# Optimization experiments

Hardware: AMD Instinct MI355X
Metric: run time of the kernel (lower is better)

The kernel has to match this reference:

```python
import jax, jax.numpy as jnp
import numpy as np

N_NODES = 50000


def setup_inputs() -> dict:
    key = jax.random.key(0)
    k1, k2, k3, k4, k5 = jax.random.split(key, 5)
    d_in, d_out, n_edges = 128, 128, 800000
    x = jax.random.normal(k1, (N_NODES, d_in), dtype=jnp.float32)
    edge_index = jax.random.randint(k2, (2, n_edges), 0, N_NODES, dtype=jnp.int64)
    # Glorot-ish init for linear weights, bias zeros-like small normal
    W_l = jax.random.normal(k3, (d_in, d_out), dtype=jnp.float32) / np.sqrt(d_in)
    W_r = jax.random.normal(k4, (d_in, d_out), dtype=jnp.float32) / np.sqrt(d_in)
    b = jax.random.normal(k5, (d_out,), dtype=jnp.float32) * 0.01
    return {"x": x, "edge_index": edge_index, "W_l": W_l, "W_r": W_r, "b": b}


def reference(x, edge_index, W_l, W_r, b):
    # PyG SAGEConv (aggr='mean', root_weight=True, bias=True):
    #   out_i = W_l @ mean_{j: (j->i) in E} x_j + b + W_r @ x_i
    # followed by ReLU (GConv act) and dropout(p=0.0, eval) == identity.
    src, dst = edge_index[0], edge_index[1]
    msgs = x[src]                                            # [E, d_in] gather
    agg_sum = jax.ops.segment_sum(msgs, dst, num_segments=N_NODES)  # [N, d_in]
    deg = jax.ops.segment_sum(jnp.ones_like(dst, dtype=x.dtype), dst,
                              num_segments=N_NODES)          # [N]
    agg_mean = agg_sum / jnp.maximum(deg, 1.0)[:, None]      # zero for isolated nodes
    z = agg_mean @ W_l + b + x @ W_r                         # [N, d_out]
    return jax.nn.relu(z)
```

## Files before the change

### kernel.cpp

```cpp
#include <hip/hip_runtime.h>

#define N_NODES 50000
#define D 128
#define NC 256
#define SCANB 196
#define CONV_NB 1563

typedef short bf16x8 __attribute__((ext_vector_type(8)));
typedef float f32x4 __attribute__((ext_vector_type(4)));
typedef float f32x2 __attribute__((ext_vector_type(2)));
typedef unsigned char uchar;

__device__ __forceinline__ ushort f2bf(float f) {
    uint u = __float_as_uint(f);
    u += 0x7FFF + ((u >> 16) & 1);
    return (ushort)(u >> 16);
}

__device__ __forceinline__ void addrow8(uint2 q, float* a) {
    f32x2 p;
    p = __builtin_amdgcn_cvt_pk_f32_fp8(q.x, false); a[0] += p.x; a[1] += p.y;
    p = __builtin_amdgcn_cvt_pk_f32_fp8(q.x, true);  a[2] += p.x; a[3] += p.y;
    p = __builtin_amdgcn_cvt_pk_f32_fp8(q.y, false); a[4] += p.x; a[5] += p.y;
    p = __builtin_amdgcn_cvt_pk_f32_fp8(q.y, true);  a[6] += p.x; a[7] += p.y;
}

__device__ __forceinline__ void scan_base(const int* __restrict__ blocksums,
                                          int* base, int* wtot) {
    const int t = threadIdx.x;
    const int lane = t & 63;
    const int wid = t >> 6;
    int v = (t < SCANB) ? blocksums[t] : 0;
    int sc = v;
    #pragma unroll
    for (int off = 1; off < 64; off <<= 1) {
        int u = __shfl_up(sc, off);
        if (lane >= off) sc += u;
    }
    if (t < 256 && lane == 63) wtot[wid] = sc;
    __syncthreads();
    if (t < SCANB) {
        int wb = 0;
        #pragma unroll
        for (int w2 = 0; w2 < 4; ++w2) if (w2 < wid) wb += wtot[w2];
        base[t] = wb + sc - v;
    }
    __syncthreads();
}

__global__ __launch_bounds__(1024) void fused_count_convert(
        const float* __restrict__ x, const float* __restrict__ Wl,
        const float* __restrict__ Wr, const int* __restrict__ dst,
        ushort* __restrict__ x_bf, int* __restrict__ x_fp8,
        ushort* __restrict__ Btf, uchar* __restrict__ cum,
        int E, int chunk) {
    const int b = blockIdx.x;
    const int t = threadIdx.x;
    if (b < NC) {
        __shared__ uint cnt[N_NODES / 4];
        for (int k = t; k < N_NODES / 4; k += 1024) cnt[k] = 0;
        __syncthreads();
        const int e0 = b * chunk;
        const int e1 = min(E, e0 + chunk);
        for (int e = e0 + t; e < e1; e += 1024) {
            int d = dst[e];
            atomicAdd(&cnt[d >> 2], 1u << ((d & 3) << 3));
        }
        __syncthreads();
        uint* pu = (uint*)(cum + (size_t)b * N_NODES);
        for (int k = t; k < N_NODES / 4; k += 1024) pu[k] = cnt[k];
    } else {
        const int i = (b - NC) * 1024 + t;
        if (i < (N_NODES * D) / 4) {
            float4 v = ((const float4*)x)[i];
            ushort4 o;
            o.x = f2bf(v.x); o.y = f2bf(v.y); o.z = f2bf(v.z); o.w = f2bf(v.w);
            ((ushort4*)x_bf)[i] = o;
            int p = __builtin_amdgcn_cvt_pk_fp8_f32(v.x, v.y, 0, false);
            p = __builtin_amdgcn_cvt_pk_fp8_f32(v.z, v.w, p, true);
            x_fp8[i] = p;
        }
        if (i < 32768) {
            int j  = i & 7;
            int l  = (i >> 3) & 63;
            int nf = (i >> 9) & 7;
            int ks = (i >> 12) & 7;
            int lr = l & 15, kb = l >> 4;
            int col  = nf * 16 + lr;
            int kloc = (ks & 3) * 32 + kb * 8 + j;
            const float* W = (ks < 4) ? Wl : Wr;
            Btf[i] = f2bf(W[kloc * D + col]);
        }
    }
}

__global__ __launch_bounds__(256) void scanAB_kernel(uchar* __restrict__ cum,
                                                     int* __restrict__ offsets,
                                                     int* __restrict__ blocksums) {
    __shared__ int wsums[4];
    __shared__ int wbase[4];
    const int t = threadIdx.x;
    const int lane = t & 63;
    const int wid = t >> 6;
    const int n = blockIdx.x * 256 + t;

    int s = 0;
    if (n < N_NODES) {
        #pragma unroll 4
        for (int c = 0; c < NC; ++c) {
            int v = (int)cum[(size_t)c * N_NODES + n];
            cum[(size_t)c * N_NODES + n] = (uchar)s;
            s += v;
        }
    }
    int sc = s;
    #pragma unroll
    for (int off = 1; off < 64; off <<= 1) {
        int u = __shfl_up(sc, off);
        if (lane >= off) sc += u;
    }
    if (lane == 63) wsums[wid] = sc;
    __syncthreads();
    if (t == 0) {
        int c = 0;
        #pragma unroll
        for (int w = 0; w < 4; ++w) { int tmp = wsums[w]; wbase[w] = c; c += tmp; }
        blocksums[blockIdx.x] = c;
    }
    __syncthreads();
    if (n < N_NODES) offsets[n] = wbase[wid] + sc - s;
}

__global__ __launch_bounds__(1024) void scatterC_kernel(const int* __restrict__ src,
                                                        const int* __restrict__ dst,
                                                        const int* __restrict__ offsets,
                                                        const int* __restrict__ blocksums,
                                                        const uchar* __restrict__ cum,
                                                        ushort* __restrict__ sorted_src,
                                                        int E, int chunk) {
    __shared__ uint cnt[N_NODES / 4];
    __shared__ int base[SCANB];
    __shared__ int wtot[4];
    const int t = threadIdx.x;
    const int b = blockIdx.x;
    for (int k = t; k < N_NODES / 4; k += 1024) cnt[k] = 0;
    scan_base(blocksums, base, wtot);
    const uchar* cb = cum + (size_t)b * N_NODES;
    const int e0 = b * chunk;
    const int e1 = min(E, e0 + chunk);
    for (int e = e0 + t; e < e1; e += 1024) {
        int d = dst[e];
        uint prev = atomicAdd(&cnt[d >> 2], 1u << ((d & 3) << 3));
        int lrank = (int)((prev >> ((d & 3) << 3)) & 0xFFu);
        int pos = offsets[d] + base[d >> 8] + (int)cb[d] + lrank;
        sorted_src[pos] = (ushort)src[e];
    }
}

__global__ __launch_bounds__(256) void aggregate_fp8(const int* __restrict__ x_fp8,
                                                     const ushort* __restrict__ sorted_src,
                                                     const int* __restrict__ offsets,
                                                     const int* __restrict__ blocksums,
                                                     ushort* __restrict__ agg_bf, int E) {
    __shared__ int base[SCANB];
    __shared__ int wtot[4];
    const int b = blockIdx.x;
    const int t = threadIdx.x;

    scan_base(blocksums, base, wtot);

    const int g = t >> 4;
    const int j = t & 15;
    const int node = b * 16 + g;
    if (node >= N_NODES) return;
    const int s = offsets[node] + base[node >> 8];
    const int np = node + 1;
    const int e = (np < N_NODES) ? (offsets[np] + base[np >> 8]) : E;

    const uint2* xq = (const uint2*)x_fp8;

    float a[8];
    #pragma unroll
    for (int k = 0; k < 8; ++k) a[k] = 0.0f;

    int p = s;
    for (; p + 8 <= e; p += 8) {
        int s0 = sorted_src[p + 0];
        int s1 = sorted_src[p + 1];
        int s2 = sorted_src[p + 2];
        int s3 = sorted_src[p + 3];
        int s4 = sorted_src[p + 4];
        int s5 = sorted_src[p + 5];
        int s6 = sorted_src[p + 6];
        int s7 = sorted_src[p + 7];
        uint2 q0 = xq[s0 * 16 + j];
        uint2 q1 = xq[s1 * 16 + j];
        uint2 q2 = xq[s2 * 16 + j];
        uint2 q3 = xq[s3 * 16 + j];
        uint2 q4 = xq[s4 * 16 + j];
        uint2 q5 = xq[s5 * 16 + j];
        uint2 q6 = xq[s6 * 16 + j];
        uint2 q7 = xq[s7 * 16 + j];
        addrow8(q0, a); addrow8(q1, a); addrow8(q2, a); addrow8(q3, a);
        addrow8(q4, a); addrow8(q5, a); addrow8(q6, a); addrow8(q7, a);
    }
    for (; p < e; ++p) {
        int s0 = sorted_src[p];
        uint2 q0 = xq[s0 * 16 + j];
        addrow8(q0, a);
    }

    const int dcnt = e - s;
    const float scale = (dcnt > 0) ? (1.0f / (float)dcnt) : 0.0f;
    ushort tmp[8];
    #pragma unroll
    for (int k = 0; k < 8; ++k) tmp[k] = f2bf(a[k] * scale);
    *(int4*)&agg_bf[node * D + j * 8] = *(int4*)tmp;
}

__global__ __launch_bounds__(256) void gemm_direct(const ushort* __restrict__ agg_bf,
                                                   const ushort* __restrict__ x_bf,
                                                   const ushort* __restrict__ Btf,
                                                   const float* __restrict__ bias,
                                                   float* __restrict__ out) {
    const int t = threadIdx.x;
    const int w = t >> 6;
    const int l = t & 63;
    const int lr = l & 15;
    const int kb = l >> 4;
    const int n0 = blockIdx.x * 64;

    int r = n0 + w * 16 + lr;
    if (r >= N_NODES) r = N_NODES - 1;

    f32x4 acc[8] = {};

    #pragma unroll
    for (int ks = 0; ks < 8; ++ks) {
        bf16x8 af = (ks < 4)
            ? *(const bf16x8*)&agg_bf[r * D + ks * 32 + kb * 8]
            : *(const bf16x8*)&x_bf[r * D + (ks - 4) * 32 + kb * 8];
        const ushort* bp = Btf + (size_t)(ks * 8 * 64 + l) * 8;
        #pragma unroll
        for (int nf = 0; nf < 8; ++nf) {
            bf16x8 bfr = *(const bf16x8*)&bp[nf * 64 * 8];
            acc[nf] = __builtin_amdgcn_mfma_f32_16x16x32_bf16(af, bfr, acc[nf], 0, 0, 0);
        }
    }

    #pragma unroll
    for (int nf = 0; nf < 8; ++nf) {
        const int col = nf * 16 + lr;
        const float bb = bias[col];
        #pragma unroll
        for (int i = 0; i < 4; ++i) {
            int row = n0 + w * 16 + kb * 4 + i;
            if (row < N_NODES)
                out[row * D + col] = fmaxf(acc[nf][i] + bb, 0.0f);
        }
    }
}

extern "C" void kernel_launch(void* const* d_in, const int* in_sizes, int n_in,
                              void* d_out, int out_size, void* d_ws, size_t ws_size,
                              hipStream_t stream) {
    const float* x  = (const float*)d_in[0];
    const int*   ei = (const int*)d_in[1];
    const float* Wl = (const float*)d_in[2];
    const float* Wr = (const float*)d_in[3];
    const float* b  = (const float*)d_in[4];
    float* out = (float*)d_out;

    const int E = in_sizes[1] / 2;
    const int* src = ei;
    const int* dst = ei + E;
    const int chunk = (E + NC - 1) / NC;

    char* wsp = (char*)d_ws;
    int*    offsets   = (int*)(wsp + 0);
    int*    blocksums = (int*)(wsp + 200704);
    ushort* sorted    = (ushort*)(wsp + 201728);
    uchar*  cum       = (uchar*)(wsp + 1801760);
    ushort* x_bf      = (ushort*)(wsp + 14601760);
    int*    x_fp8     = (int*)(wsp + 27401760);
    ushort* agg_bf    = (ushort*)(wsp + 33801760);
    ushort* Btf       = (ushort*)(wsp + 46601760);

    fused_count_convert<<<NC + CONV_NB, 1024, 0, stream>>>(
        x, Wl, Wr, dst, x_bf, x_fp8, Btf, cum, E, chunk);
    scanAB_kernel<<<SCANB, 256, 0, stream>>>(cum, offsets, blocksums);
    scatterC_kernel<<<NC, 1024, 0, stream>>>(src, dst, offsets, blocksums, cum,
                                             sorted, E, chunk);
    aggregate_fp8<<<(N_NODES + 15) / 16, 256, 0, stream>>>(
        x_fp8, sorted, offsets, blocksums, agg_bf, E);
    gemm_direct<<<(N_NODES + 63) / 64, 256, 0, stream>>>(agg_bf, x_bf, Btf, b, out);
}
```

Before: 98.45 us.

## Pad per-node edge segments to multiples of 8 with zero-row sentinel

Each node's segment in the sorted source array is rounded up to a multiple of 8. Unused slots are pre-filled with the index of an added all-zero fp8 row, and a per-node degree array is kept. The aggregation loop then reads 8 source indices with one 16-byte load and drops the scalar tail loop, with degree taken from the stored count. The cost is extra gathers of the zero row, a larger sorted buffer to fill, and an extra degree write in the scan.

```diff
diff --git a/kernel.cpp b/kernel.cpp
--- a/kernel.cpp
+++ b/kernel.cpp
@@ -5,6 +5,7 @@
 #define NC 256
 #define SCANB 196
 #define CONV_NB 1563
+#define ZROW 50000
 
 typedef short bf16x8 __attribute__((ext_vector_type(8)));
 typedef float f32x4 __attribute__((ext_vector_type(4)));
@@ -53,6 +54,7 @@
         const float* __restrict__ Wr, const int* __restrict__ dst,
         ushort* __restrict__ x_bf, int* __restrict__ x_fp8,
         ushort* __restrict__ Btf, uchar* __restrict__ cum,
+        uint* __restrict__ sorted_u32,
         int E, int chunk) {
     const int b = blockIdx.x;
     const int t = threadIdx.x;
@@ -80,6 +82,8 @@
             p = __builtin_amdgcn_cvt_pk_fp8_f32(v.z, v.w, p, true);
             x_fp8[i] = p;
         }
+        if (i < 600008) sorted_u32[i] = 0xC350C350u;
+        if (i < 32) x_fp8[ZROW * 32 + i] = 0;
         if (i < 32768) {
             int j  = i & 7;
             int l  = (i >> 3) & 63;
@@ -95,8 +99,9 @@
 }
 
 __global__ __launch_bounds__(256) void scanAB_kernel(uchar* __restrict__ cum,
-                                                     int* __restrict__ offsets,
-                                                     int* __restrict__ blocksums) {
+                                                     int* __restrict__ offsetsP,
+                                                     int* __restrict__ blocksums,
+                                                     ushort* __restrict__ degArr) {
     __shared__ int wsums[4];
     __shared__ int wbase[4];
     const int t = threadIdx.x;
@@ -112,8 +117,10 @@
             cum[(size_t)c * N_NODES + n] = (uchar)s;
             s += v;
         }
-    }
-    int sc = s;
+        degArr[n] = (ushort)s;
+    }
+    const int sp = (s + 7) & ~7;
+    int sc = sp;
     #pragma unroll
     for (int off = 1; off < 64; off <<= 1) {
         int u = __shfl_up(sc, off);
@@ -128,12 +135,12 @@
         blocksums[blockIdx.x] = c;
     }
     __syncthreads();
-    if (n < N_NODES) offsets[n] = wbase[wid] + sc - s;
+    if (n < N_NODES) offsetsP[n] = wbase[wid] + sc - sp;
 }
 
 __global__ __launch_bounds__(1024) void scatterC_kernel(const int* __restrict__ src,
                                                         const int* __restrict__ dst,
-                                                        const int* __restrict__ offsets,
+                                                        const int* __restrict__ offsetsP,
                                                         const int* __restrict__ blocksums,
                                                         const uchar* __restrict__ cum,
                                                         ushort* __restrict__ sorted_src,
@@ -152,16 +159,17 @@
         int d = dst[e];
         uint prev = atomicAdd(&cnt[d >> 2], 1u << ((d & 3) << 3));
         int lrank = (int)((prev >> ((d & 3) << 3)) & 0xFFu);
-        int pos = offsets[d] + base[d >> 8] + (int)cb[d] + lrank;
+        int pos = offsetsP[d] + base[d >> 8] + (int)cb[d] + lrank;
         sorted_src[pos] = (ushort)src[e];
     }
 }
 
 __global__ __launch_bounds__(256) void aggregate_fp8(const int* __restrict__ x_fp8,
                                                      const ushort* __restrict__ sorted_src,
-                                                     const int* __restrict__ offsets,
+                                                     const int* __restrict__ offsetsP,
                                                      const int* __restrict__ blocksums,
-                                                     ushort* __restrict__ agg_bf, int E) {
+                                                     const ushort* __restrict__ degArr,
+                                                     ushort* __restrict__ agg_bf) {
     __shared__ int base[SCANB];
     __shared__ int wtot[4];
     const int b = blockIdx.x;
@@ -173,9 +181,9 @@
     const int j = t & 15;
     const int node = b * 16 + g;
     if (node >= N_NODES) return;
-    const int s = offsets[node] + base[node >> 8];
-    const int np = node + 1;
-    const int e = (np < N_NODES) ? (offsets[np] + base[np >> 8]) : E;
+    const int dg = (int)degArr[node];
+    const int s = offsetsP[node] + base[node >> 8];
+    const int npad = (dg + 7) & ~7;
 
     const uint2* xq = (const uint2*)x_fp8;
 
@@ -183,16 +191,13 @@
     #pragma unroll
     for (int k = 0; k < 8; ++k) a[k] = 0.0f;
 
-    int p = s;
-    for (; p + 8 <= e; p += 8) {
-        int s0 = sorted_src[p + 0];
-        int s1 = sorted_src[p + 1];
-        int s2 = sorted_src[p + 2];
-        int s3 = sorted_src[p + 3];
-        int s4 = sorted_src[p + 4];
-        int s5 = sorted_src[p + 5];
-        int s6 = sorted_src[p + 6];
-        int s7 = sorted_src[p + 7];
+    const int pend = s + npad;
+    for (int p = s; p < pend; p += 8) {
+        uint4 qi = *(const uint4*)&sorted_src[p];
+        int s0 = qi.x & 0xFFFF, s1 = qi.x >> 16;
+        int s2 = qi.y & 0xFFFF, s3 = qi.y >> 16;
+        int s4 = qi.z & 0xFFFF, s5 = qi.z >> 16;
+        int s6 = qi.w & 0xFFFF, s7 = qi.w >> 16;
         uint2 q0 = xq[s0 * 16 + j];
         uint2 q1 = xq[s1 * 16 + j];
         uint2 q2 = xq[s2 * 16 + j];
@@ -204,14 +209,8 @@
         addrow8(q0, a); addrow8(q1, a); addrow8(q2, a); addrow8(q3, a);
         addrow8(q4, a); addrow8(q5, a); addrow8(q6, a); addrow8(q7, a);
     }
-    for (; p < e; ++p) {
-        int s0 = sorted_src[p];
-        uint2 q0 = xq[s0 * 16 + j];
-        addrow8(q0, a);
-    }
-
-    const int dcnt = e - s;
-    const float scale = (dcnt > 0) ? (1.0f / (float)dcnt) : 0.0f;
+
+    const float scale = (dg > 0) ? (1.0f / (float)dg) : 0.0f;
     ushort tmp[8];
     #pragma unroll
     for (int k = 0; k < 8; ++k) tmp[k] = f2bf(a[k] * scale);
@@ -277,21 +276,22 @@
     const int chunk = (E + NC - 1) / NC;
 
     char* wsp = (char*)d_ws;
-    int*    offsets   = (int*)(wsp + 0);
+    int*    offsetsP  = (int*)(wsp + 0);
     int*    blocksums = (int*)(wsp + 200704);
-    ushort* sorted    = (ushort*)(wsp + 201728);
-    uchar*  cum       = (uchar*)(wsp + 1801760);
-    ushort* x_bf      = (ushort*)(wsp + 14601760);
-    int*    x_fp8     = (int*)(wsp + 27401760);
-    ushort* agg_bf    = (ushort*)(wsp + 33801760);
-    ushort* Btf       = (ushort*)(wsp + 46601760);
+    ushort* degArr    = (ushort*)(wsp + 201728);
+    ushort* sorted    = (ushort*)(wsp + 301760);
+    uchar*  cum       = (uchar*)(wsp + 2701792);
+    ushort* x_bf      = (ushort*)(wsp + 15501792);
+    int*    x_fp8     = (int*)(wsp + 28301792);
+    ushort* agg_bf    = (ushort*)(wsp + 34701920);
+    ushort* Btf       = (ushort*)(wsp + 47501920);
 
     fused_count_convert<<<NC + CONV_NB, 1024, 0, stream>>>(
-        x, Wl, Wr, dst, x_bf, x_fp8, Btf, cum, E, chunk);
-    scanAB_kernel<<<SCANB, 256, 0, stream>>>(cum, offsets, blocksums);
-    scatterC_kernel<<<NC, 1024, 0, stream>>>(src, dst, offsets, blocksums, cum,
+        x, Wl, Wr, dst, x_bf, x_fp8, Btf, cum, (uint*)sorted, E, chunk);
+    scanAB_kernel<<<SCANB, 256, 0, stream>>>(cum, offsetsP, blocksums, degArr);
+    scatterC_kernel<<<NC, 1024, 0, stream>>>(src, dst, offsetsP, blocksums, cum,
                                              sorted, E, chunk);
     aggregate_fp8<<<(N_NODES + 15) / 16, 256, 0, stream>>>(
-        x_fp8, sorted, offsets, blocksums, agg_bf, E);
+        x_fp8, sorted, offsetsP, blocksums, degArr, agg_bf);
     gemm_direct<<<(N_NODES + 63) / 64, 256, 0, stream>>>(agg_bf, x_bf, Btf, b, out);
 }
```

Result: faster. 96.36 us (median of 2 runs) (-2.1%).
